# Kernel optimization log

Measured on AMD Instinct MI355X. Metric: run time of the kernel, lower is better.

## Reference

```python
import jax, jax.numpy as jnp
import numpy as np

B, S = 4096, 256
D = 32  # output_size // 4


def setup_inputs() -> dict:
    key = jax.random.key(0)
    ks = jax.random.split(key, 32)
    # continuous features
    cont_p = jax.random.normal(ks[0], (B, S, 3), dtype=jnp.float32)
    cont_c = jax.random.normal(ks[1], (B, S, 2), dtype=jnp.float32)
    # categorical features, per-column vocab sizes from Embedding tables
    vocabs_p = [2, 2, 2, 11, 34]
    cat_p = jnp.stack([
        jax.random.randint(ks[2 + i], (B, S), 0, v, dtype=jnp.int32)
        for i, v in enumerate(vocabs_p)], axis=2)
    vocabs_c = [19, 31]
    cat_c = jnp.stack([
        jax.random.randint(ks[7 + i], (B, S), 0, v, dtype=jnp.int32)
        for i, v in enumerate(vocabs_c)], axis=2)
    lengths = jax.random.randint(ks[9], (B,), 1, S + 1, dtype=jnp.int32)

    def lin(k, fan_in, fan_out):
        bound = 1.0 / np.sqrt(fan_in)
        kw, kb = jax.random.split(k)
        w = jax.random.uniform(kw, (fan_in, fan_out), jnp.float32, -bound, bound)
        b = jax.random.uniform(kb, (fan_out,), jnp.float32, -bound, bound)
        return w, b

    w_p1, b_p1 = lin(ks[10], 3, D)
    w_p2, b_p2 = lin(ks[11], D, D)
    w_c1, b_c1 = lin(ks[12], 2, D)
    w_c2, b_c2 = lin(ks[13], D, D)
    emb_gender = jax.random.normal(ks[14], (2, D), dtype=jnp.float32)
    emb_korean = jax.random.normal(ks[15], (2, D), dtype=jnp.float32)
    emb_primary = jax.random.normal(ks[16], (2, D), dtype=jnp.float32)
    emb_job = jax.random.normal(ks[17], (11, D), dtype=jnp.float32)
    emb_rep = jax.random.normal(ks[18], (34, D), dtype=jnp.float32)
    emb_place = jax.random.normal(ks[19], (19, D), dtype=jnp.float32)
    emb_add = jax.random.normal(ks[20], (31, D), dtype=jnp.float32)
    w_fc1, b_fc1 = lin(ks[21], 128, 64)
    w_fc2, b_fc2 = lin(ks[22], 64, 2)

    return dict(cont_p=cont_p, cont_c=cont_c, cat_p=cat_p, cat_c=cat_c,
                lengths=lengths,
                w_p1=w_p1, b_p1=b_p1, w_p2=w_p2, b_p2=b_p2,
                w_c1=w_c1, b_c1=b_c1, w_c2=w_c2, b_c2=b_c2,
                emb_gender=emb_gender, emb_korean=emb_korean,
                emb_primary=emb_primary, emb_job=emb_job, emb_rep=emb_rep,
                emb_place=emb_place, emb_add=emb_add,
                w_fc1=w_fc1, b_fc1=b_fc1, w_fc2=w_fc2, b_fc2=b_fc2)


def reference(cont_p, cont_c, cat_p, cat_c, lengths,
              w_p1, b_p1, w_p2, b_p2, w_c1, b_c1, w_c2, b_c2,
              emb_gender, emb_korean, emb_primary, emb_job, emb_rep,
              emb_place, emb_add, w_fc1, b_fc1, w_fc2, b_fc2):
    # small per-token MLPs on continuous features -> [B,S,D]
    hp = jax.nn.relu(cont_p @ w_p1 + b_p1) @ w_p2 + b_p2
    hc = jax.nn.relu(cont_c @ w_c1 + b_c1) @ w_c2 + b_c2
    # multi-table embedding lookups, averaged per group -> [B,S,D]
    ep = (emb_gender[cat_p[:, :, 0]] + emb_korean[cat_p[:, :, 1]] +
          emb_primary[cat_p[:, :, 2]] + emb_job[cat_p[:, :, 3]] +
          emb_rep[cat_p[:, :, 4]]) / 5.0
    ec = (emb_place[cat_c[:, :, 0]] + emb_add[cat_c[:, :, 1]]) / 2.0
    # concat order matches torch: (cat_p, cat_c, cont_p, cont_c) -> [B,S,128]
    x = jnp.concatenate([ep, ec, hp, hc], axis=2)
    # ragged mean pool over first lengths[i] positions (masked segment mean)
    mask = (jnp.arange(x.shape[1])[None, :] < lengths[:, None])
    pooled = jnp.sum(x * mask[:, :, None], axis=1) / lengths[:, None].astype(x.dtype)
    # head: relu(fc1) -> relu(fc2); dropout p=0.0 is identity
    h = jax.nn.relu(pooled @ w_fc1 + b_fc1)
    return jax.nn.relu(h @ w_fc2 + b_fc2)
```

## Files before the change

### kernel.cpp

```cpp
#include <hip/hip_runtime.h>


#define BDIM 512

__global__ __launch_bounds__(BDIM, 1)
void mlpreg_kernel(const float* __restrict__ cont_p,
                   const float* __restrict__ cont_c,
                   const int* __restrict__ cat_p,
                   const int* __restrict__ cat_c,
                   const int* __restrict__ lengths,
                   const float* __restrict__ w_p1, const float* __restrict__ b_p1,
                   const float* __restrict__ w_p2, const float* __restrict__ b_p2,
                   const float* __restrict__ w_c1, const float* __restrict__ b_c1,
                   const float* __restrict__ w_c2, const float* __restrict__ b_c2,
                   const float* __restrict__ emb_g,  const float* __restrict__ emb_k,
                   const float* __restrict__ emb_pr, const float* __restrict__ emb_j,
                   const float* __restrict__ emb_r,  const float* __restrict__ emb_pl,
                   const float* __restrict__ emb_a,
                   const float* __restrict__ w_fc1, const float* __restrict__ b_fc1,
                   const float* __restrict__ w_fc2, const float* __restrict__ b_fc2,
                   float* __restrict__ out)
{
    constexpr int S = 256;
    __shared__ float sPc[16 * 768];
    __shared__ float sCc[16 * 512];
    __shared__ float sW1[128 * 64];
    __shared__ float sAcc[16][64];
    __shared__ float sPB[16 * 128];

    const int tid  = threadIdx.x;
    const int wid  = tid >> 6;
    const int lane = tid & 63;
    const int ch   = lane & 31, h = lane >> 5;
    const int lr0  = wid << 1;
    const int b0   = blockIdx.x * 16 + lr0, b1 = b0 + 1;

    int L0 = lengths[b0]; L0 = (L0 < 1) ? 1 : (L0 > S ? S : L0);
    int L1 = lengths[b1]; L1 = (L1 < 1) ? 1 : (L1 > S ? S : L1);
    const float L0f = (float)L0, L1f = (float)L1;
    const float invL0 = 1.0f / L0f, invL1 = 1.0f / L1f;

    const float wp0 = w_p1[ch], wp1 = w_p1[32 + ch], wp2 = w_p1[64 + ch], bp = b_p1[ch];
    const float wc0 = w_c1[ch], wc1 = w_c1[32 + ch], bc = b_c1[ch];
    const float eg0 = emb_g[ch],  eg1 = emb_g[32 + ch];
    const float ek0 = emb_k[ch],  ek1 = emb_k[32 + ch];
    const float er0 = emb_pr[ch], er1 = emb_pr[32 + ch];
    const float bias2 = h ? b_c2[ch] : b_p2[ch];
    const float bf1 = b_fc1[lane];
    const float2 wf2 = *(const float2*)&w_fc2[2 * lane];
    const float bq0 = b_fc2[0], bq1 = b_fc2[1];

    {
        const float4* gp0 = (const float4*)(cont_p + (size_t)b0 * 768);
        const float4* gp1 = (const float4*)(cont_p + (size_t)b1 * 768);
        const float4* gc0 = (const float4*)(cont_c + (size_t)b0 * 512);
        const float4* gc1 = (const float4*)(cont_c + (size_t)b1 * 512);
        float4* dp0 = (float4*)(sPc + lr0 * 768);
        float4* dp1 = (float4*)(sPc + (lr0 + 1) * 768);
        float4* dc0 = (float4*)(sCc + lr0 * 512);
        float4* dc1 = (float4*)(sCc + (lr0 + 1) * 512);
        const int n0 = (3 * L0 + 3) >> 2, n1 = (3 * L1 + 3) >> 2;
        const int m0 = (L0 + 1) >> 1,     m1 = (L1 + 1) >> 1;
        for (int i = lane; i < n0; i += 64) dp0[i] = gp0[i];
        for (int i = lane; i < n1; i += 64) dp1[i] = gp1[i];
        for (int i = lane; i < m0; i += 64) dc0[i] = gc0[i];
        for (int i = lane; i < m1; i += 64) dc1[i] = gc1[i];
    }
    {
        const float4* gw = (const float4*)w_fc1;
        float4* dw = (float4*)sW1;
        #pragma unroll
        for (int i = tid; i < 2048; i += BDIM) dw[i] = gw[i];
    }
    int* hist0 = (int*)(sPB + lr0 * 128);
    int* hist1 = (int*)(sPB + (lr0 + 1) * 128);
    hist0[lane] = 0; hist1[lane] = 0;
    if (lane < 32) { hist0[64 + lane] = 0; hist1[64 + lane] = 0; }

    int sg0 = 0, sk0 = 0, sp0 = 0, sg1 = 0, sk1 = 0, sp1 = 0;
    {
        const int*  kp0 = cat_p + (size_t)b0 * (S * 5);
        const int*  kp1 = cat_p + (size_t)b1 * (S * 5);
        const int2* kc0 = (const int2*)(cat_c + (size_t)b0 * (S * 2));
        const int2* kc1 = (const int2*)(cat_c + (size_t)b1 * (S * 2));
        #pragma unroll 2
        for (int t = lane; t < L0; t += 64) {
            int v0 = kp0[5 * t], v1 = kp0[5 * t + 1], v2 = kp0[5 * t + 2],
                v3 = kp0[5 * t + 3], v4 = kp0[5 * t + 4];
            int2 q = kc0[t];
            sg0 += v0; sk0 += v1; sp0 += v2;
            atomicAdd(&hist0[v3], 1);
            atomicAdd(&hist0[11 + v4], 1);
            atomicAdd(&hist0[45 + q.x], 1);
            atomicAdd(&hist0[64 + q.y], 1);
        }
        #pragma unroll 2
        for (int t = lane; t < L1; t += 64) {
            int v0 = kp1[5 * t], v1 = kp1[5 * t + 1], v2 = kp1[5 * t + 2],
                v3 = kp1[5 * t + 3], v4 = kp1[5 * t + 4];
            int2 q = kc1[t];
            sg1 += v0; sk1 += v1; sp1 += v2;
            atomicAdd(&hist1[v3], 1);
            atomicAdd(&hist1[11 + v4], 1);
            atomicAdd(&hist1[45 + q.x], 1);
            atomicAdd(&hist1[64 + q.y], 1);
        }
    }
    #pragma unroll
    for (int d = 32; d; d >>= 1) {
        sg0 += __shfl_xor(sg0, d); sk0 += __shfl_xor(sk0, d); sp0 += __shfl_xor(sp0, d);
        sg1 += __shfl_xor(sg1, d); sk1 += __shfl_xor(sk1, d); sp1 += __shfl_xor(sp1, d);
    }
    __syncthreads();

    {
        const int   lr   = lr0 + h;
        const int   Lr   = h ? L1 : L0;
        const float invr = h ? invL1 : invL0;
        const float* tp = sPc + lr * 768;
        const float* tc = sCc + lr * 512;
        float aP = 0.f, aC = 0.f;
        #pragma unroll 4
        for (int t = 0; t < Lr; ++t) {
            float c0 = tp[3 * t], c1 = tp[3 * t + 1], c2 = tp[3 * t + 2];
            float2 d2 = *(const float2*)&tc[2 * t];
            aP += fmaxf(fmaf(c0, wp0, fmaf(c1, wp1, fmaf(c2, wp2, bp))), 0.f);
            aC += fmaxf(fmaf(d2.x, wc0, fmaf(d2.y, wc1, bc)), 0.f);
        }
        sAcc[lr][ch]      = aP * invr;
        sAcc[lr][32 + ch] = aC * invr;
    }

    float A0, A1;
    {
        float fg0 = (float)sg0, fk0 = (float)sk0, fp0 = (float)sp0;
        float fg1 = (float)sg1, fk1 = (float)sk1, fp1 = (float)sp1;
        A0 = fmaf(L0f - fg0, eg0, fg0 * eg1) + fmaf(L0f - fk0, ek0, fk0 * ek1)
           + fmaf(L0f - fp0, er0, fp0 * er1);
        A1 = fmaf(L1f - fg1, eg0, fg1 * eg1) + fmaf(L1f - fk1, ek0, fk1 * ek1)
           + fmaf(L1f - fp1, er0, fp1 * er1);
        if (h) { A0 = 0.f; A1 = 0.f; }
    }
    {
        const float* tA = h ? emb_pl : emb_j;
        const float* tB = h ? emb_a  : emb_r;
        const int nA = h ? 19 : 11;
        const int nT = h ? 50 : 45;
        const int hb = h ? 45 : 0;
        #pragma unroll 5
        for (int r = 0; r < nT; ++r) {
            const float* p = (r < nA) ? (tA + (r << 5)) : (tB + ((r - nA) << 5));
            float w = p[ch];
            A0 = fmaf((float)hist0[hb + r], w, A0);
            A1 = fmaf((float)hist1[hb + r], w, A1);
        }
        const float sc = h ? 0.5f : 0.2f;
        sPB[lr0 * 128 + (h << 5) + ch]       = A0 * (invL0 * sc);
        sPB[(lr0 + 1) * 128 + (h << 5) + ch] = A1 * (invL1 * sc);
    }
    {
        const float* W2 = h ? w_c2 : w_p2;
        const float* a0 = &sAcc[lr0][h << 5];
        const float* a1 = &sAcc[lr0 + 1][h << 5];
        float v0 = bias2, v1 = bias2;
        #pragma unroll 8
        for (int k = 0; k < 32; ++k) {
            float w = W2[(k << 5) + ch];
            v0 = fmaf(a0[k], w, v0);
            v1 = fmaf(a1[k], w, v1);
        }
        sPB[lr0 * 128 + 64 + (h << 5) + ch]       = v0;
        sPB[(lr0 + 1) * 128 + 64 + (h << 5) + ch] = v1;
    }

    {
        const float* P0 = sPB + lr0 * 128;
        const float* P1 = P0 + 128;
        float x0 = bf1, y0 = 0.f, x1 = bf1, y1 = 0.f;
        #pragma unroll 8
        for (int k = 0; k < 128; k += 2) {
            float w0 = sW1[k * 64 + lane];
            float w1 = sW1[(k + 1) * 64 + lane];
            float2 u0 = *(const float2*)&P0[k];
            float2 u1 = *(const float2*)&P1[k];
            x0 = fmaf(u0.x, w0, x0); y0 = fmaf(u0.y, w1, y0);
            x1 = fmaf(u1.x, w0, x1); y1 = fmaf(u1.y, w1, y1);
        }
        float h0v = fmaxf(x0 + y0, 0.f);
        float h1v = fmaxf(x1 + y1, 0.f);
        float q00 = h0v * wf2.x, q01 = h0v * wf2.y;
        float q10 = h1v * wf2.x, q11 = h1v * wf2.y;
        #pragma unroll
        for (int d = 32; d; d >>= 1) {
            q00 += __shfl_xor(q00, d); q01 += __shfl_xor(q01, d);
            q10 += __shfl_xor(q10, d); q11 += __shfl_xor(q11, d);
        }
        if (lane == 0) {
            float4 o4;
            o4.x = fmaxf(q00 + bq0, 0.f);
            o4.y = fmaxf(q01 + bq1, 0.f);
            o4.z = fmaxf(q10 + bq0, 0.f);
            o4.w = fmaxf(q11 + bq1, 0.f);
            *(float4*)&out[(size_t)b0 * 2] = o4;
        }
    }
}

extern "C" void kernel_launch(void* const* d_in, const int* in_sizes, int n_in,
                              void* d_out, int out_size, void* d_ws, size_t ws_size,
                              hipStream_t stream) {
    const float* cont_p = (const float*)d_in[0];
    const float* cont_c = (const float*)d_in[1];
    const int*   cat_p  = (const int*)d_in[2];
    const int*   cat_c  = (const int*)d_in[3];
    const int*   lens   = (const int*)d_in[4];
    const float* w_p1   = (const float*)d_in[5];
    const float* b_p1   = (const float*)d_in[6];
    const float* w_p2   = (const float*)d_in[7];
    const float* b_p2   = (const float*)d_in[8];
    const float* w_c1   = (const float*)d_in[9];
    const float* b_c1   = (const float*)d_in[10];
    const float* w_c2   = (const float*)d_in[11];
    const float* b_c2   = (const float*)d_in[12];
    const float* emb_g  = (const float*)d_in[13];
    const float* emb_k  = (const float*)d_in[14];
    const float* emb_pr = (const float*)d_in[15];
    const float* emb_j  = (const float*)d_in[16];
    const float* emb_r  = (const float*)d_in[17];
    const float* emb_pl = (const float*)d_in[18];
    const float* emb_a  = (const float*)d_in[19];
    const float* w_fc1  = (const float*)d_in[20];
    const float* b_fc1  = (const float*)d_in[21];
    const float* w_fc2  = (const float*)d_in[22];
    const float* b_fc2  = (const float*)d_in[23];
    float* out = (float*)d_out;

    hipLaunchKernelGGL(mlpreg_kernel, dim3(256), dim3(BDIM), 0, stream,
                       cont_p, cont_c, cat_p, cat_c, lens,
                       w_p1, b_p1, w_p2, b_p2, w_c1, b_c1, w_c2, b_c2,
                       emb_g, emb_k, emb_pr, emb_j, emb_r, emb_pl, emb_a,
                       w_fc1, b_fc1, w_fc2, b_fc2, out);
}
```

Measured before the change: 143.2 us.

## Use one-wave blocks per row pair, stream inputs from global without LDS staging

Replaces 512-thread blocks with 64-thread single-wavefront blocks, each handling two batch rows, and launches 2048 blocks instead of 256. The big shared-memory staging buffers for continuous features and fc1 weights are removed. Continuous features are read directly as float4 groups, categorical indices are preloaded as int4 vectors, and fc1 weights come straight from global memory. This is meant to raise occupancy and remove the staging copies and long-latency serial phases, at the cost of more redundant global and L2 reads of the shared weights.

Result: slower. 153.2 us (+6.9%).

```diff
diff --git a/kernel.cpp b/kernel.cpp
--- a/kernel.cpp
+++ b/kernel.cpp
@@ -1,9 +1,9 @@
 #include <hip/hip_runtime.h>
 
 
-#define BDIM 512
-
-__global__ __launch_bounds__(BDIM, 1)
+#define BDIM 64
+
+__global__ __launch_bounds__(BDIM, 2)
 void mlpreg_kernel(const float* __restrict__ cont_p,
                    const float* __restrict__ cont_c,
                    const int* __restrict__ cat_p,
@@ -22,18 +22,13 @@
                    float* __restrict__ out)
 {
     constexpr int S = 256;
-    __shared__ float sPc[16 * 768];
-    __shared__ float sCc[16 * 512];
-    __shared__ float sW1[128 * 64];
-    __shared__ float sAcc[16][64];
-    __shared__ float sPB[16 * 128];
-
-    const int tid  = threadIdx.x;
-    const int wid  = tid >> 6;
-    const int lane = tid & 63;
-    const int ch   = lane & 31, h = lane >> 5;
-    const int lr0  = wid << 1;
-    const int b0   = blockIdx.x * 16 + lr0, b1 = b0 + 1;
+    __shared__ int   hist[2][96];
+    __shared__ float sAcc[2][64];
+    __shared__ float sPool[2][128];
+
+    const int lane = threadIdx.x;
+    const int ch = lane & 31, h = lane >> 5;
+    const int b0 = blockIdx.x * 2, b1 = b0 + 1;
 
     int L0 = lengths[b0]; L0 = (L0 < 1) ? 1 : (L0 > S ? S : L0);
     int L1 = lengths[b1]; L1 = (L1 < 1) ? 1 : (L1 > S ? S : L1);
@@ -50,60 +45,112 @@
     const float2 wf2 = *(const float2*)&w_fc2[2 * lane];
     const float bq0 = b_fc2[0], bq1 = b_fc2[1];
 
-    {
-        const float4* gp0 = (const float4*)(cont_p + (size_t)b0 * 768);
-        const float4* gp1 = (const float4*)(cont_p + (size_t)b1 * 768);
-        const float4* gc0 = (const float4*)(cont_c + (size_t)b0 * 512);
-        const float4* gc1 = (const float4*)(cont_c + (size_t)b1 * 512);
-        float4* dp0 = (float4*)(sPc + lr0 * 768);
-        float4* dp1 = (float4*)(sPc + (lr0 + 1) * 768);
-        float4* dc0 = (float4*)(sCc + lr0 * 512);
-        float4* dc1 = (float4*)(sCc + (lr0 + 1) * 512);
-        const int n0 = (3 * L0 + 3) >> 2, n1 = (3 * L1 + 3) >> 2;
-        const int m0 = (L0 + 1) >> 1,     m1 = (L1 + 1) >> 1;
-        for (int i = lane; i < n0; i += 64) dp0[i] = gp0[i];
-        for (int i = lane; i < n1; i += 64) dp1[i] = gp1[i];
-        for (int i = lane; i < m0; i += 64) dc0[i] = gc0[i];
-        for (int i = lane; i < m1; i += 64) dc1[i] = gc1[i];
-    }
-    {
-        const float4* gw = (const float4*)w_fc1;
-        float4* dw = (float4*)sW1;
-        #pragma unroll
-        for (int i = tid; i < 2048; i += BDIM) dw[i] = gw[i];
-    }
-    int* hist0 = (int*)(sPB + lr0 * 128);
-    int* hist1 = (int*)(sPB + (lr0 + 1) * 128);
-    hist0[lane] = 0; hist1[lane] = 0;
-    if (lane < 32) { hist0[64 + lane] = 0; hist1[64 + lane] = 0; }
+    { int i = lane;  ((int*)hist)[i] = 0;
+      i += 64;       ((int*)hist)[i] = 0;
+      i += 64;       ((int*)hist)[i] = 0; }
+
+    const int4* KP0 = (const int4*)(cat_p + (size_t)b0 * (S * 5));
+    const int4* KP1 = (const int4*)(cat_p + (size_t)b1 * (S * 5));
+    const int4* KC0 = (const int4*)(cat_c + (size_t)b0 * (S * 2));
+    const int4* KC1 = (const int4*)(cat_c + (size_t)b1 * (S * 2));
+    const int lim_p0 = 5 * L0, lim_p1 = 5 * L1;
+    const int lim_c0 = 2 * L0, lim_c1 = 2 * L1;
+    int4 qp0[5], qp1[5], qc0[2], qc1[2];
+    #pragma unroll
+    for (int j = 0; j < 5; ++j) {
+        if (256 * j < lim_p0) qp0[j] = KP0[lane + 64 * j];
+        if (256 * j < lim_p1) qp1[j] = KP1[lane + 64 * j];
+    }
+    #pragma unroll
+    for (int j = 0; j < 2; ++j) {
+        if (256 * j < lim_c0) qc0[j] = KC0[lane + 64 * j];
+        if (256 * j < lim_c1) qc1[j] = KC1[lane + 64 * j];
+    }
+
+    {
+        const int   row  = h ? b1 : b0;
+        const int   Lr   = h ? L1 : L0;
+        const float invr = h ? invL1 : invL0;
+        const float4* tp4 = (const float4*)(cont_p + (size_t)row * 768);
+        const float4* tc4 = (const float4*)(cont_c + (size_t)row * 512);
+        float aP = 0.f, aC = 0.f;
+        const int gf = Lr >> 2;
+        #pragma unroll 4
+        for (int g = 0; g < gf; ++g) {
+            float4 a  = tp4[3 * g], bb = tp4[3 * g + 1], cc = tp4[3 * g + 2];
+            float4 d  = tc4[2 * g], ee = tc4[2 * g + 1];
+            float p0 = fmaxf(fmaf(a.x,  wp0, fmaf(a.y,  wp1, fmaf(a.z,  wp2, bp))), 0.f);
+            float p1 = fmaxf(fmaf(a.w,  wp0, fmaf(bb.x, wp1, fmaf(bb.y, wp2, bp))), 0.f);
+            float p2 = fmaxf(fmaf(bb.z, wp0, fmaf(bb.w, wp1, fmaf(cc.x, wp2, bp))), 0.f);
+            float p3 = fmaxf(fmaf(cc.y, wp0, fmaf(cc.z, wp1, fmaf(cc.w, wp2, bp))), 0.f);
+            aP += (p0 + p1) + (p2 + p3);
+            float q0 = fmaxf(fmaf(d.x,  wc0, fmaf(d.y,  wc1, bc)), 0.f);
+            float q1 = fmaxf(fmaf(d.z,  wc0, fmaf(d.w,  wc1, bc)), 0.f);
+            float q2 = fmaxf(fmaf(ee.x, wc0, fmaf(ee.y, wc1, bc)), 0.f);
+            float q3 = fmaxf(fmaf(ee.z, wc0, fmaf(ee.w, wc1, bc)), 0.f);
+            aC += (q0 + q1) + (q2 + q3);
+        }
+        const int rem = Lr & 3;
+        if (rem) {
+            const float* tp = (const float*)(tp4 + 3 * gf);
+            const float* tc = (const float*)(tc4 + 2 * gf);
+            for (int r = 0; r < rem; ++r) {
+                aP += fmaxf(fmaf(tp[3*r], wp0, fmaf(tp[3*r+1], wp1, fmaf(tp[3*r+2], wp2, bp))), 0.f);
+                aC += fmaxf(fmaf(tc[2*r], wc0, fmaf(tc[2*r+1], wc1, bc)), 0.f);
+            }
+        }
+        sAcc[h][ch]      = aP * invr;
+        sAcc[h][32 + ch] = aC * invr;
+    }
 
     int sg0 = 0, sk0 = 0, sp0 = 0, sg1 = 0, sk1 = 0, sp1 = 0;
-    {
-        const int*  kp0 = cat_p + (size_t)b0 * (S * 5);
-        const int*  kp1 = cat_p + (size_t)b1 * (S * 5);
-        const int2* kc0 = (const int2*)(cat_c + (size_t)b0 * (S * 2));
-        const int2* kc1 = (const int2*)(cat_c + (size_t)b1 * (S * 2));
-        #pragma unroll 2
-        for (int t = lane; t < L0; t += 64) {
-            int v0 = kp0[5 * t], v1 = kp0[5 * t + 1], v2 = kp0[5 * t + 2],
-                v3 = kp0[5 * t + 3], v4 = kp0[5 * t + 4];
-            int2 q = kc0[t];
-            sg0 += v0; sk0 += v1; sp0 += v2;
-            atomicAdd(&hist0[v3], 1);
-            atomicAdd(&hist0[11 + v4], 1);
-            atomicAdd(&hist0[45 + q.x], 1);
-            atomicAdd(&hist0[64 + q.y], 1);
-        }
-        #pragma unroll 2
-        for (int t = lane; t < L1; t += 64) {
-            int v0 = kp1[5 * t], v1 = kp1[5 * t + 1], v2 = kp1[5 * t + 2],
-                v3 = kp1[5 * t + 3], v4 = kp1[5 * t + 4];
-            int2 q = kc1[t];
-            sg1 += v0; sk1 += v1; sp1 += v2;
-            atomicAdd(&hist1[v3], 1);
-            atomicAdd(&hist1[11 + v4], 1);
-            atomicAdd(&hist1[45 + q.x], 1);
-            atomicAdd(&hist1[64 + q.y], 1);
+    const int m0 = (lane << 2) % 5;
+    #pragma unroll
+    for (int j = 0; j < 5; ++j) {
+        int mj = m0 + j; if (mj >= 5) mj -= 5;
+        if (256 * j < lim_p0) {
+            const int base = 4 * lane + 256 * j;
+            const int v[4] = {qp0[j].x, qp0[j].y, qp0[j].z, qp0[j].w};
+            #pragma unroll
+            for (int c = 0; c < 4; ++c) {
+                int f = mj + c; if (f >= 5) f -= 5;
+                const bool val = (base + c) < lim_p0;
+                const int vv = v[c];
+                sg0 += (val && f == 0) ? vv : 0;
+                sk0 += (val && f == 1) ? vv : 0;
+                sp0 += (val && f == 2) ? vv : 0;
+                if (val && f >= 3) atomicAdd(&hist[0][(f == 4 ? 11 : 0) + vv], 1);
+            }
+        }
+        if (256 * j < lim_p1) {
+            const int base = 4 * lane + 256 * j;
+            const int v[4] = {qp1[j].x, qp1[j].y, qp1[j].z, qp1[j].w};
+            #pragma unroll
+            for (int c = 0; c < 4; ++c) {
+                int f = mj + c; if (f >= 5) f -= 5;
+                const bool val = (base + c) < lim_p1;
+                const int vv = v[c];
+                sg1 += (val && f == 0) ? vv : 0;
+                sk1 += (val && f == 1) ? vv : 0;
+                sp1 += (val && f == 2) ? vv : 0;
+                if (val && f >= 3) atomicAdd(&hist[1][(f == 4 ? 11 : 0) + vv], 1);
+            }
+        }
+    }
+    #pragma unroll
+    for (int j = 0; j < 2; ++j) {
+        const int base = 4 * lane + 256 * j;
+        if (256 * j < lim_c0) {
+            if (base     < lim_c0) atomicAdd(&hist[0][45 + qc0[j].x], 1);
+            if (base + 1 < lim_c0) atomicAdd(&hist[0][64 + qc0[j].y], 1);
+            if (base + 2 < lim_c0) atomicAdd(&hist[0][45 + qc0[j].z], 1);
+            if (base + 3 < lim_c0) atomicAdd(&hist[0][64 + qc0[j].w], 1);
+        }
+        if (256 * j < lim_c1) {
+            if (base     < lim_c1) atomicAdd(&hist[1][45 + qc1[j].x], 1);
+            if (base + 1 < lim_c1) atomicAdd(&hist[1][64 + qc1[j].y], 1);
+            if (base + 2 < lim_c1) atomicAdd(&hist[1][45 + qc1[j].z], 1);
+            if (base + 3 < lim_c1) atomicAdd(&hist[1][64 + qc1[j].w], 1);
         }
     }
     #pragma unroll
@@ -112,24 +159,6 @@
         sg1 += __shfl_xor(sg1, d); sk1 += __shfl_xor(sk1, d); sp1 += __shfl_xor(sp1, d);
     }
     __syncthreads();
-
-    {
-        const int   lr   = lr0 + h;
-        const int   Lr   = h ? L1 : L0;
-        const float invr = h ? invL1 : invL0;
-        const float* tp = sPc + lr * 768;
-        const float* tc = sCc + lr * 512;
-        float aP = 0.f, aC = 0.f;
-        #pragma unroll 4
-        for (int t = 0; t < Lr; ++t) {
-            float c0 = tp[3 * t], c1 = tp[3 * t + 1], c2 = tp[3 * t + 2];
-            float2 d2 = *(const float2*)&tc[2 * t];
-            aP += fmaxf(fmaf(c0, wp0, fmaf(c1, wp1, fmaf(c2, wp2, bp))), 0.f);
-            aC += fmaxf(fmaf(d2.x, wc0, fmaf(d2.y, wc1, bc)), 0.f);
-        }
-        sAcc[lr][ch]      = aP * invr;
-        sAcc[lr][32 + ch] = aC * invr;
-    }
 
     float A0, A1;
     {
@@ -151,17 +180,17 @@
         for (int r = 0; r < nT; ++r) {
             const float* p = (r < nA) ? (tA + (r << 5)) : (tB + ((r - nA) << 5));
             float w = p[ch];
-            A0 = fmaf((float)hist0[hb + r], w, A0);
-            A1 = fmaf((float)hist1[hb + r], w, A1);
+            A0 = fmaf((float)hist[0][hb + r], w, A0);
+            A1 = fmaf((float)hist[1][hb + r], w, A1);
         }
         const float sc = h ? 0.5f : 0.2f;
-        sPB[lr0 * 128 + (h << 5) + ch]       = A0 * (invL0 * sc);
-        sPB[(lr0 + 1) * 128 + (h << 5) + ch] = A1 * (invL1 * sc);
+        sPool[0][(h << 5) + ch] = A0 * (invL0 * sc);
+        sPool[1][(h << 5) + ch] = A1 * (invL1 * sc);
     }
     {
         const float* W2 = h ? w_c2 : w_p2;
-        const float* a0 = &sAcc[lr0][h << 5];
-        const float* a1 = &sAcc[lr0 + 1][h << 5];
+        const float* a0 = &sAcc[0][h << 5];
+        const float* a1 = &sAcc[1][h << 5];
         float v0 = bias2, v1 = bias2;
         #pragma unroll 8
         for (int k = 0; k < 32; ++k) {
@@ -169,18 +198,19 @@
             v0 = fmaf(a0[k], w, v0);
             v1 = fmaf(a1[k], w, v1);
         }
-        sPB[lr0 * 128 + 64 + (h << 5) + ch]       = v0;
-        sPB[(lr0 + 1) * 128 + 64 + (h << 5) + ch] = v1;
-    }
-
-    {
-        const float* P0 = sPB + lr0 * 128;
-        const float* P1 = P0 + 128;
+        sPool[0][64 + (h << 5) + ch] = v0;
+        sPool[1][64 + (h << 5) + ch] = v1;
+    }
+    __syncthreads();
+
+    {
+        const float* P0 = sPool[0];
+        const float* P1 = sPool[1];
         float x0 = bf1, y0 = 0.f, x1 = bf1, y1 = 0.f;
         #pragma unroll 8
         for (int k = 0; k < 128; k += 2) {
-            float w0 = sW1[k * 64 + lane];
-            float w1 = sW1[(k + 1) * 64 + lane];
+            float w0 = w_fc1[(size_t)k * 64 + lane];
+            float w1 = w_fc1[(size_t)(k + 1) * 64 + lane];
             float2 u0 = *(const float2*)&P0[k];
             float2 u1 = *(const float2*)&P1[k];
             x0 = fmaf(u0.x, w0, x0); y0 = fmaf(u0.y, w1, y0);
@@ -235,7 +265,7 @@
     const float* b_fc2  = (const float*)d_in[23];
     float* out = (float*)d_out;
 
-    hipLaunchKernelGGL(mlpreg_kernel, dim3(256), dim3(BDIM), 0, stream,
+    hipLaunchKernelGGL(mlpreg_kernel, dim3(2048), dim3(BDIM), 0, stream,
                        cont_p, cont_c, cat_p, cat_c, lens,
                        w_p1, b_p1, w_p2, b_p2, w_c1, b_c1, w_c2, b_c2,
                        emb_g, emb_k, emb_pr, emb_j, emb_r, emb_pl, emb_a,
```
